# Performance work log

Hardware: AMD Instinct MI355X
Metric: run time of the kernel (lower is better)

## Reference

```python
import jax, jax.numpy as jnp
import numpy as np

N0_SRC, N0_DST, E0 = 495616, 45056, 450560
N1_DST, E1 = 4096, 40960
IN_FEATS, N_HIDDEN, N_CLASSES = 256, 128, 16


def setup_inputs() -> dict:
    key = jax.random.key(0)
    ks = jax.random.split(key, 12)
    x = jax.random.normal(ks[0], (N0_SRC, IN_FEATS), dtype=jnp.float32)
    src0 = jax.random.randint(ks[1], (E0,), 0, N0_SRC, dtype=jnp.int32)
    dst0 = jax.random.randint(ks[2], (E0,), 0, N0_DST, dtype=jnp.int32)
    w0 = jax.random.uniform(ks[3], (E0,), dtype=jnp.float32)
    src1 = jax.random.randint(ks[4], (E1,), 0, N0_DST, dtype=jnp.int32)
    dst1 = jax.random.randint(ks[5], (E1,), 0, N1_DST, dtype=jnp.int32)
    w1 = jax.random.uniform(ks[6], (E1,), dtype=jnp.float32)
    # xavier-uniform-ish init for linear weights
    def xavier(k, shape):
        fan_out, fan_in = shape
        lim = jnp.sqrt(6.0 / (fan_in + fan_out))
        return jax.random.uniform(k, shape, jnp.float32, -lim, lim)
    return {
        "x": x, "src0": src0, "dst0": dst0, "w0": w0,
        "src1": src1, "dst1": dst1, "w1": w1,
        "Wn0": xavier(ks[7], (N_HIDDEN, IN_FEATS)), "bn0": jnp.zeros((N_HIDDEN,), jnp.float32),
        "Wn1": xavier(ks[8], (N_HIDDEN, N_HIDDEN)), "bn1": jnp.zeros((N_HIDDEN,), jnp.float32),
        "Wfc": xavier(ks[9], (N_CLASSES, N_HIDDEN)), "bfc": jnp.zeros((N_CLASSES,), jnp.float32),
        "ndst0": N0_DST, "ndst1": N1_DST,
    }


def _weighted_sage_gcn(h, src, dst, w, Wn, bn, num_dst):
    """DGL-style 'gcn' SAGEConv with edge weights on a bipartite block.

    dst nodes are the prefix h[:num_dst] of the src node set.
    h_out = relu(fc_neigh((sum_e w_e*h[src_e] + h_dst) / (sum_e w_e + 1)))
    """
    h_dst = h[:num_dst]
    msg = h[src] * w[:, None]                                   # [E, D]
    agg = jax.ops.segment_sum(msg, dst, num_segments=num_dst)   # [num_dst, D]
    deg = jax.ops.segment_sum(w, dst, num_segments=num_dst)     # [num_dst]
    h_neigh = (agg + h_dst) / (deg[:, None] + 1.0)
    return jax.nn.relu(h_neigh @ Wn.T + bn)


def reference(x, src0, dst0, w0, src1, dst1, w1, Wn0, bn0, Wn1, bn1, Wfc, bfc, ndst0, ndst1):
    h = _weighted_sage_gcn(x, src0, dst0, w0, Wn0, bn0, ndst0)
    h = _weighted_sage_gcn(h, src1, dst1, w1, Wn1, bn1, ndst1)
    return h @ Wfc.T + bfc  # [ndst1, n_classes]
```

## Files before the change

### kernel.cpp

```cpp
#include <hip/hip_runtime.h>

#define N0_SRC 495616
#define N0_DST 45056
#define E0 450560
#define N1_DST 4096
#define E1 40960
#define IN_FEATS 256
#define NH 128
#define NC 16

__global__ void hist_kernel(const int* __restrict__ dst, int* __restrict__ cnt) {
    int e = blockIdx.x * blockDim.x + threadIdx.x;
    if (e < E0) atomicAdd(&cnt[dst[e]], 1);
}

__global__ void __launch_bounds__(1024) scan_kernel(int* __restrict__ cnt,
                                                    int* __restrict__ row_start) {
    __shared__ int partial[1024];
    const int CH = N0_DST / 1024;
    int t = threadIdx.x;
    int base = t * CH;
    int s = 0;
    for (int j = 0; j < CH; j++) s += cnt[base + j];
    partial[t] = s;
    __syncthreads();
    for (int off = 1; off < 1024; off <<= 1) {
        int v = (t >= off) ? partial[t - off] : 0;
        __syncthreads();
        partial[t] += v;
        __syncthreads();
    }
    int run = partial[t] - s;
    for (int j = 0; j < CH; j++) {
        int c = cnt[base + j];
        row_start[base + j] = run;
        cnt[base + j] = run;
        run += c;
    }
    if (t == 1023) row_start[N0_DST] = run;
}

__global__ void scatter_kernel(const int* __restrict__ dst, int* __restrict__ cursor,
                               int* __restrict__ perm) {
    int e = blockIdx.x * blockDim.x + threadIdx.x;
    if (e < E0) {
        int p = atomicAdd(&cursor[dst[e]], 1);
        perm[p] = e;
    }
}

__global__ void __launch_bounds__(256) agg0_kernel(const float* __restrict__ x,
    const int* __restrict__ src0, const float* __restrict__ w0,
    const int* __restrict__ perm, const int* __restrict__ row_start,
    float* __restrict__ hneigh) {
    int wv = blockIdx.x * 4 + (threadIdx.x >> 6);
    int lane = threadIdx.x & 63;
    if (wv >= N0_DST) return;
    int beg = row_start[wv], end = row_start[wv + 1];
    const float4* x4 = (const float4*)x;
    float4 acc = make_float4(0.f, 0.f, 0.f, 0.f);
    float degs = 0.f;
    int s = 0; float we = 0.f;
    if (beg < end) { int e = perm[beg]; s = src0[e]; we = w0[e]; }
    for (int i = beg; i < end; i++) {
        int s2 = 0; float we2 = 0.f;
        if (i + 1 < end) { int e2 = perm[i + 1]; s2 = src0[e2]; we2 = w0[e2]; }
        float4 v = x4[(size_t)s * 64 + lane];
        acc.x += we * v.x; acc.y += we * v.y; acc.z += we * v.z; acc.w += we * v.w;
        degs += we;
        s = s2; we = we2;
    }
    float4 xd = x4[(size_t)wv * 64 + lane];
    float inv = 1.0f / (degs + 1.0f);
    float4 r;
    r.x = (acc.x + xd.x) * inv; r.y = (acc.y + xd.y) * inv;
    r.z = (acc.z + xd.z) * inv; r.w = (acc.w + xd.w) * inv;
    ((float4*)hneigh)[(size_t)wv * 64 + lane] = r;
}

__global__ void __launch_bounds__(128) gemm0_kernel(const float* __restrict__ hneigh,
    const float* __restrict__ Wn, const float* __restrict__ bn,
    float* __restrict__ h0) {
    __shared__ float hn[8][IN_FEATS];
    int nb = blockIdx.x * 8;
    int tid = threadIdx.x;
    for (int i = tid; i < 8 * IN_FEATS; i += 128) {
        int n = i >> 8;
        int k = i & 255;
        hn[n][k] = hneigh[(size_t)(nb + n) * IN_FEATS + k];
    }
    __syncthreads();
    float acc[8];
#pragma unroll
    for (int n = 0; n < 8; n++) acc[n] = 0.f;
    const float4* wr4 = (const float4*)(Wn + (size_t)tid * IN_FEATS);
#pragma unroll 4
    for (int k4 = 0; k4 < IN_FEATS / 4; k4++) {
        float4 wv = wr4[k4];
        int k = k4 * 4;
#pragma unroll
        for (int n = 0; n < 8; n++) {
            acc[n] += hn[n][k + 0] * wv.x;
            acc[n] += hn[n][k + 1] * wv.y;
            acc[n] += hn[n][k + 2] * wv.z;
            acc[n] += hn[n][k + 3] * wv.w;
        }
    }
    float b = bn[tid];
#pragma unroll
    for (int n = 0; n < 8; n++) {
        float v = acc[n] + b;
        h0[(size_t)(nb + n) * NH + tid] = v > 0.f ? v : 0.f;
    }
}

__global__ void edge1_kernel(const float* __restrict__ h0,
                             const int* __restrict__ src, const int* __restrict__ dst,
                             const float* __restrict__ w,
                             float* __restrict__ agg, float* __restrict__ deg) {
    int t = blockIdx.x * blockDim.x + threadIdx.x;
    int e = t >> 5;
    int lane = t & 31;
    if (e >= E1) return;
    int s = src[e], d = dst[e];
    float we = w[e];
    float4 v = ((const float4*)(h0 + (size_t)s * NH))[lane];
    float* ad = agg + (size_t)d * NH + lane * 4;
    unsafeAtomicAdd(ad + 0, v.x * we);
    unsafeAtomicAdd(ad + 1, v.y * we);
    unsafeAtomicAdd(ad + 2, v.z * we);
    unsafeAtomicAdd(ad + 3, v.w * we);
    if (lane == 0) unsafeAtomicAdd(deg + d, we);
}

__global__ void __launch_bounds__(128) gemm1_kernel(const float* __restrict__ h0,
    const float* __restrict__ agg, const float* __restrict__ deg,
    const float* __restrict__ Wn, const float* __restrict__ bn,
    float* __restrict__ h1) {
    __shared__ float hn[8][NH];
    int nb = blockIdx.x * 8;
    int tid = threadIdx.x;
    for (int i = tid; i < 8 * NH; i += 128) {
        int n = i >> 7;
        int k = i & 127;
        int m = nb + n;
        float hv = agg[(size_t)m * NH + k] + h0[(size_t)m * NH + k];
        hn[n][k] = hv / (deg[m] + 1.0f);
    }
    __syncthreads();
    float acc[8];
#pragma unroll
    for (int n = 0; n < 8; n++) acc[n] = 0.f;
    const float4* wr4 = (const float4*)(Wn + (size_t)tid * NH);
#pragma unroll 4
    for (int k4 = 0; k4 < NH / 4; k4++) {
        float4 wv = wr4[k4];
        int k = k4 * 4;
#pragma unroll
        for (int n = 0; n < 8; n++) {
            acc[n] += hn[n][k + 0] * wv.x;
            acc[n] += hn[n][k + 1] * wv.y;
            acc[n] += hn[n][k + 2] * wv.z;
            acc[n] += hn[n][k + 3] * wv.w;
        }
    }
    float b = bn[tid];
#pragma unroll
    for (int n = 0; n < 8; n++) {
        float v = acc[n] + b;
        h1[(size_t)(nb + n) * NH + tid] = v > 0.f ? v : 0.f;
    }
}

__global__ void fc_kernel(const float* __restrict__ h1, const float* __restrict__ Wfc,
                          const float* __restrict__ bfc, float* __restrict__ out) {
    int t = blockIdx.x * blockDim.x + threadIdx.x;
    int m = t >> 4, c = t & 15;
    if (m >= N1_DST) return;
    const float* hr = h1 + (size_t)m * NH;
    const float* wr = Wfc + (size_t)c * NH;
    float acc = 0.f;
    for (int k = 0; k < NH; k++) acc += hr[k] * wr[k];
    out[t] = acc + bfc[c];
}

extern "C" void kernel_launch(void* const* d_in, const int* in_sizes, int n_in,
                              void* d_out, int out_size, void* d_ws, size_t ws_size,
                              hipStream_t stream) {
    const float* x   = (const float*)d_in[0];
    const int* src0  = (const int*)d_in[1];
    const int* dst0  = (const int*)d_in[2];
    const float* w0  = (const float*)d_in[3];
    const int* src1  = (const int*)d_in[4];
    const int* dst1  = (const int*)d_in[5];
    const float* w1  = (const float*)d_in[6];
    const float* Wn0 = (const float*)d_in[7];
    const float* bn0 = (const float*)d_in[8];
    const float* Wn1 = (const float*)d_in[9];
    const float* bn1 = (const float*)d_in[10];
    const float* Wfc = (const float*)d_in[11];
    const float* bfc = (const float*)d_in[12];
    float* out = (float*)d_out;

    float* ws = (float*)d_ws;
    float* agg1      = ws;
    float* deg1      = agg1 + (size_t)N1_DST * NH;
    int*   cnt       = (int*)(deg1 + N1_DST);
    int*   row_start = cnt + N0_DST;
    int*   perm      = row_start + N0_DST + 1;
    float* hneigh    = (float*)(perm + E0);
    float* h0        = hneigh + (size_t)N0_DST * IN_FEATS;
    float* h1        = (float*)cnt;

    size_t zero_floats = (size_t)N1_DST * NH + N1_DST + N0_DST;
    hipMemsetAsync(d_ws, 0, zero_floats * sizeof(float), stream);

    hist_kernel<<<(E0 + 255) / 256, 256, 0, stream>>>(dst0, cnt);
    scan_kernel<<<1, 1024, 0, stream>>>(cnt, row_start);
    scatter_kernel<<<(E0 + 255) / 256, 256, 0, stream>>>(dst0, cnt, perm);

    agg0_kernel<<<(N0_DST + 3) / 4, 256, 0, stream>>>(x, src0, w0, perm, row_start, hneigh);
    gemm0_kernel<<<N0_DST / 8, 128, 0, stream>>>(hneigh, Wn0, bn0, h0);

    edge1_kernel<<<(E1 * 32) / 256, 256, 0, stream>>>(h0, src1, dst1, w1, agg1, deg1);
    gemm1_kernel<<<N1_DST / 8, 128, 0, stream>>>(h0, agg1, deg1, Wn1, bn1, h1);

    fc_kernel<<<(N1_DST * NC) / 256, 256, 0, stream>>>(h1, Wfc, bfc, out);
}
```

Before: 955.5 us.

## Use register-tiled 128x128 shared-memory GEMMs and prefetch gathered rows in agg0

Both dense layers are rewritten as 128x128 block tiles, with 256 threads each computing an 8x8 register tile from shared-memory At/Wt tiles staged in K chunks of 32. This replaces the old 8-row-per-block kernels, which reread the weight matrix for every 8 nodes and did little register reuse. In the layer-1 GEMM the normalisation (agg+h0)/(deg+1) is folded into the tile load. The agg0 loop now also software-prefetches the next neighbour's feature float4 as well as its index, to hide gather latency. The cost is higher register pressure and fewer blocks in the smaller layer-1 GEMM.

```diff
diff --git a/kernel.cpp b/kernel.cpp
--- a/kernel.cpp
+++ b/kernel.cpp
@@ -60,15 +60,21 @@
     const float4* x4 = (const float4*)x;
     float4 acc = make_float4(0.f, 0.f, 0.f, 0.f);
     float degs = 0.f;
-    int s = 0; float we = 0.f;
-    if (beg < end) { int e = perm[beg]; s = src0[e]; we = w0[e]; }
-    for (int i = beg; i < end; i++) {
-        int s2 = 0; float we2 = 0.f;
-        if (i + 1 < end) { int e2 = perm[i + 1]; s2 = src0[e2]; we2 = w0[e2]; }
+    if (beg < end) {
+        int e = perm[beg];
+        int s = src0[e];
+        float we = w0[e];
         float4 v = x4[(size_t)s * 64 + lane];
-        acc.x += we * v.x; acc.y += we * v.y; acc.z += we * v.z; acc.w += we * v.w;
-        degs += we;
-        s = s2; we = we2;
+        for (int i = beg; i < end; i++) {
+            int s2 = 0; float we2 = 0.f;
+            if (i + 1 < end) { int e2 = perm[i + 1]; s2 = src0[e2]; we2 = w0[e2]; }
+            float4 vn = v;
+            if (i + 1 < end) vn = x4[(size_t)s2 * 64 + lane];
+            acc.x += we * v.x; acc.y += we * v.y;
+            acc.z += we * v.z; acc.w += we * v.w;
+            degs += we;
+            v = vn; we = we2;
+        }
     }
     float4 xd = x4[(size_t)wv * 64 + lane];
     float inv = 1.0f / (degs + 1.0f);
@@ -78,39 +84,64 @@
     ((float4*)hneigh)[(size_t)wv * 64 + lane] = r;
 }
 
-__global__ void __launch_bounds__(128) gemm0_kernel(const float* __restrict__ hneigh,
-    const float* __restrict__ Wn, const float* __restrict__ bn,
-    float* __restrict__ h0) {
-    __shared__ float hn[8][IN_FEATS];
-    int nb = blockIdx.x * 8;
-    int tid = threadIdx.x;
-    for (int i = tid; i < 8 * IN_FEATS; i += 128) {
-        int n = i >> 8;
-        int k = i & 255;
-        hn[n][k] = hneigh[(size_t)(nb + n) * IN_FEATS + k];
-    }
-    __syncthreads();
-    float acc[8];
-#pragma unroll
-    for (int n = 0; n < 8; n++) acc[n] = 0.f;
-    const float4* wr4 = (const float4*)(Wn + (size_t)tid * IN_FEATS);
-#pragma unroll 4
-    for (int k4 = 0; k4 < IN_FEATS / 4; k4++) {
-        float4 wv = wr4[k4];
-        int k = k4 * 4;
-#pragma unroll
-        for (int n = 0; n < 8; n++) {
-            acc[n] += hn[n][k + 0] * wv.x;
-            acc[n] += hn[n][k + 1] * wv.y;
-            acc[n] += hn[n][k + 2] * wv.z;
-            acc[n] += hn[n][k + 3] * wv.w;
-        }
-    }
-    float b = bn[tid];
-#pragma unroll
-    for (int n = 0; n < 8; n++) {
-        float v = acc[n] + b;
-        h0[(size_t)(nb + n) * NH + tid] = v > 0.f ? v : 0.f;
+__global__ void __launch_bounds__(256) gemm0_v2(const float* __restrict__ A,
+    const float* __restrict__ W, const float* __restrict__ bn,
+    float* __restrict__ out) {
+    __shared__ float At[128][36];
+    __shared__ float Wt[128][36];
+    const int m0 = blockIdx.x * 128;
+    const int tx = threadIdx.x & 15;
+    const int ty = threadIdx.x >> 4;
+    const float4* A4 = (const float4*)A;
+    const float4* W4 = (const float4*)W;
+    float acc[8][8];
+#pragma unroll
+    for (int i = 0; i < 8; i++)
+#pragma unroll
+        for (int j = 0; j < 8; j++) acc[i][j] = 0.f;
+
+    for (int kc = 0; kc < IN_FEATS / 32; kc++) {
+        int kc4 = kc * 8;
+        __syncthreads();
+#pragma unroll
+        for (int q = 0; q < 4; q++) {
+            int idx = threadIdx.x + 256 * q;
+            int r = idx >> 3, c4 = idx & 7;
+            float4 v = A4[(size_t)(m0 + r) * 64 + kc4 + c4];
+            *(float4*)&At[r][c4 * 4] = v;
+            float4 wv = W4[(size_t)r * 64 + kc4 + c4];
+            *(float4*)&Wt[r][c4 * 4] = wv;
+        }
+        __syncthreads();
+#pragma unroll
+        for (int k4 = 0; k4 < 8; k4++) {
+            float4 a[8], w[8];
+#pragma unroll
+            for (int i = 0; i < 8; i++) a[i] = *(const float4*)&At[ty + 16 * i][k4 * 4];
+#pragma unroll
+            for (int j = 0; j < 8; j++) w[j] = *(const float4*)&Wt[tx + 16 * j][k4 * 4];
+#pragma unroll
+            for (int i = 0; i < 8; i++)
+#pragma unroll
+                for (int j = 0; j < 8; j++) {
+                    acc[i][j] += a[i].x * w[j].x;
+                    acc[i][j] += a[i].y * w[j].y;
+                    acc[i][j] += a[i].z * w[j].z;
+                    acc[i][j] += a[i].w * w[j].w;
+                }
+        }
+    }
+    float b[8];
+#pragma unroll
+    for (int j = 0; j < 8; j++) b[j] = bn[tx + 16 * j];
+#pragma unroll
+    for (int i = 0; i < 8; i++) {
+        size_t row = (size_t)(m0 + ty + 16 * i) * NH;
+#pragma unroll
+        for (int j = 0; j < 8; j++) {
+            float v = acc[i][j] + b[j];
+            out[row + tx + 16 * j] = v > 0.f ? v : 0.f;
+        }
     }
 }
 
@@ -133,42 +164,72 @@
     if (lane == 0) unsafeAtomicAdd(deg + d, we);
 }
 
-__global__ void __launch_bounds__(128) gemm1_kernel(const float* __restrict__ h0,
-    const float* __restrict__ agg, const float* __restrict__ deg,
-    const float* __restrict__ Wn, const float* __restrict__ bn,
-    float* __restrict__ h1) {
-    __shared__ float hn[8][NH];
-    int nb = blockIdx.x * 8;
-    int tid = threadIdx.x;
-    for (int i = tid; i < 8 * NH; i += 128) {
-        int n = i >> 7;
-        int k = i & 127;
-        int m = nb + n;
-        float hv = agg[(size_t)m * NH + k] + h0[(size_t)m * NH + k];
-        hn[n][k] = hv / (deg[m] + 1.0f);
-    }
-    __syncthreads();
-    float acc[8];
-#pragma unroll
-    for (int n = 0; n < 8; n++) acc[n] = 0.f;
-    const float4* wr4 = (const float4*)(Wn + (size_t)tid * NH);
-#pragma unroll 4
-    for (int k4 = 0; k4 < NH / 4; k4++) {
-        float4 wv = wr4[k4];
-        int k = k4 * 4;
-#pragma unroll
-        for (int n = 0; n < 8; n++) {
-            acc[n] += hn[n][k + 0] * wv.x;
-            acc[n] += hn[n][k + 1] * wv.y;
-            acc[n] += hn[n][k + 2] * wv.z;
-            acc[n] += hn[n][k + 3] * wv.w;
-        }
-    }
-    float b = bn[tid];
-#pragma unroll
-    for (int n = 0; n < 8; n++) {
-        float v = acc[n] + b;
-        h1[(size_t)(nb + n) * NH + tid] = v > 0.f ? v : 0.f;
+__global__ void __launch_bounds__(256) gemm1_v2(const float* __restrict__ agg,
+    const float* __restrict__ h0, const float* __restrict__ deg,
+    const float* __restrict__ W, const float* __restrict__ bn,
+    float* __restrict__ out) {
+    __shared__ float At[128][36];
+    __shared__ float Wt[128][36];
+    const int m0 = blockIdx.x * 128;
+    const int tx = threadIdx.x & 15;
+    const int ty = threadIdx.x >> 4;
+    const float4* G4 = (const float4*)agg;
+    const float4* H4 = (const float4*)h0;
+    const float4* W4 = (const float4*)W;
+    float acc[8][8];
+#pragma unroll
+    for (int i = 0; i < 8; i++)
+#pragma unroll
+        for (int j = 0; j < 8; j++) acc[i][j] = 0.f;
+
+    for (int kc = 0; kc < NH / 32; kc++) {
+        int kc4 = kc * 8;
+        __syncthreads();
+#pragma unroll
+        for (int q = 0; q < 4; q++) {
+            int idx = threadIdx.x + 256 * q;
+            int r = idx >> 3, c4 = idx & 7;
+            int m = m0 + r;
+            float4 g = G4[(size_t)m * 32 + kc4 + c4];
+            float4 h = H4[(size_t)m * 32 + kc4 + c4];
+            float inv = 1.0f / (deg[m] + 1.0f);
+            float4 v;
+            v.x = (g.x + h.x) * inv; v.y = (g.y + h.y) * inv;
+            v.z = (g.z + h.z) * inv; v.w = (g.w + h.w) * inv;
+            *(float4*)&At[r][c4 * 4] = v;
+            float4 wv = W4[(size_t)r * 32 + kc4 + c4];
+            *(float4*)&Wt[r][c4 * 4] = wv;
+        }
+        __syncthreads();
+#pragma unroll
+        for (int k4 = 0; k4 < 8; k4++) {
+            float4 a[8], w[8];
+#pragma unroll
+            for (int i = 0; i < 8; i++) a[i] = *(const float4*)&At[ty + 16 * i][k4 * 4];
+#pragma unroll
+            for (int j = 0; j < 8; j++) w[j] = *(const float4*)&Wt[tx + 16 * j][k4 * 4];
+#pragma unroll
+            for (int i = 0; i < 8; i++)
+#pragma unroll
+                for (int j = 0; j < 8; j++) {
+                    acc[i][j] += a[i].x * w[j].x;
+                    acc[i][j] += a[i].y * w[j].y;
+                    acc[i][j] += a[i].z * w[j].z;
+                    acc[i][j] += a[i].w * w[j].w;
+                }
+        }
+    }
+    float b[8];
+#pragma unroll
+    for (int j = 0; j < 8; j++) b[j] = bn[tx + 16 * j];
+#pragma unroll
+    for (int i = 0; i < 8; i++) {
+        size_t row = (size_t)(m0 + ty + 16 * i) * NH;
+#pragma unroll
+        for (int j = 0; j < 8; j++) {
+            float v = acc[i][j] + b[j];
+            out[row + tx + 16 * j] = v > 0.f ? v : 0.f;
+        }
     }
 }
 
@@ -220,10 +281,10 @@
     scatter_kernel<<<(E0 + 255) / 256, 256, 0, stream>>>(dst0, cnt, perm);
 
     agg0_kernel<<<(N0_DST + 3) / 4, 256, 0, stream>>>(x, src0, w0, perm, row_start, hneigh);
-    gemm0_kernel<<<N0_DST / 8, 128, 0, stream>>>(hneigh, Wn0, bn0, h0);
+    gemm0_v2<<<N0_DST / 128, 256, 0, stream>>>(hneigh, Wn0, bn0, h0);
 
     edge1_kernel<<<(E1 * 32) / 256, 256, 0, stream>>>(h0, src1, dst1, w1, agg1, deg1);
-    gemm1_kernel<<<N1_DST / 8, 128, 0, stream>>>(h0, agg1, deg1, Wn1, bn1, h1);
+    gemm1_v2<<<N1_DST / 128, 256, 0, stream>>>(agg1, h0, deg1, Wn1, bn1, h1);
 
     fc_kernel<<<(N1_DST * NC) / 256, 256, 0, stream>>>(h1, Wfc, bfc, out);
 }
```

After: 967.5 us. About the same (+1.3%).
